# Kernel tuning notes

Measured on AMD Instinct MI355X. Metric: run time of the kernel, lower is better.

Reference implementation:

```python
import jax, jax.numpy as jnp
import numpy as np

JITTER = 0.002  # original adds 0.001*I globally plus 0.001*I on each diagonal block


def setup_inputs() -> dict:
    key = jax.random.key(0)
    k1, k2, k3 = jax.random.split(key, 3)
    T, N, D, Z = 4, 1024, 64, 4
    x = jax.random.normal(k1, (T, N, D), dtype=jnp.float32)      # per-task features
    W = jax.random.normal(k2, (T, Z), dtype=jnp.float32)         # task-to-latent mixing weights
    theta = jax.random.uniform(k3, (Z, 2), dtype=jnp.float32)    # [amplitude, inv-lengthscale] per latent GP
    return {"x": x, "W": W, "theta": theta}


def reference(x, W, theta):
    # Faithful, fused version of MTGP.rbf_kernel_mo_hete with x2=None and equal
    # task lengths. cov[mi, nj] = sum_z W[task(mi),z] W[task(nj),z] * theta[z,0]
    #   * exp(-theta[z,1]/2 * ||X[mi]-X[nj]||^2)  + JITTER on the diagonal.
    T, N, D = x.shape
    Z = theta.shape[0]
    M = T * N
    X = x.reshape(M, D)
    sq = jnp.sum(X * X, axis=-1)                                  # [M]
    sqd = jnp.maximum(sq[:, None] + sq[None, :] - 2.0 * X @ X.T, 0.0)  # [M, M]
    Wexp = jnp.repeat(W, N, axis=0)                               # [M, Z] task weight per point
    cov = JITTER * jnp.eye(M, dtype=x.dtype)
    for z in range(Z):  # small fixed loop over latent GPs
        Kz = theta[z, 0] * jnp.exp(-0.5 * theta[z, 1] * sqd)      # [M, M]
        cov = cov + (Wexp[:, z][:, None] * Wexp[:, z][None, :]) * Kz
    return cov
```

## Files before the change

kernel.cpp:

```cpp
#include <hip/hip_runtime.h>


#define M_PTS 4096
#define DIM 64
#define JITTER_F 0.002f
#define NEG_HALF_LOG2E (-0.72134752044448170f)
#define NITEM 8256
#define NBLK (NITEM / 2)

typedef __attribute__((ext_vector_type(8))) short short8v;
typedef __attribute__((ext_vector_type(4))) float f32x4;

union FragU { short8v v; uint4 u; };

__device__ __forceinline__ float fast_exp2(float x) {
#if defined(__has_builtin)
#if __has_builtin(__builtin_amdgcn_exp2f)
  return __builtin_amdgcn_exp2f(x);
#else
  return exp2f(x);
#endif
#else
  return exp2f(x);
#endif
}

__device__ __forceinline__ unsigned bfr(float x) {
  unsigned u = __float_as_uint(x);
  return (u + 0x7FFFu + ((u >> 16) & 1u)) >> 16;
}
__device__ __forceinline__ float bff(unsigned h) {
  return __uint_as_float(h << 16);
}

__global__ __launch_bounds__(256) void mtgp_pack(
    const float* __restrict__ X, unsigned short* __restrict__ Ph,
    unsigned short* __restrict__ Pl, float* __restrict__ sqn) {
  const int t = blockIdx.x * 256 + threadIdx.x;
  const int row = t >> 1, k0 = t & 1;
  const float4* xr = (const float4*)(X + (size_t)row * DIM + k0 * 32);
  float va[32];
  float s = 0.0f;
#pragma unroll
  for (int i = 0; i < 8; ++i) {
    const float4 vv = xr[i];
    va[4 * i + 0] = vv.x; va[4 * i + 1] = vv.y;
    va[4 * i + 2] = vv.z; va[4 * i + 3] = vv.w;
    s = fmaf(vv.x, vv.x, s); s = fmaf(vv.y, vv.y, s);
    s = fmaf(vv.z, vv.z, s); s = fmaf(vv.w, vv.w, s);
  }
  s += __shfl_xor(s, 1);
  if (k0 == 0) sqn[row] = s;
  const int fbase = ((row >> 4) * 2 + k0) * 512;
#pragma unroll
  for (int kg = 0; kg < 4; ++kg) {
    unsigned h[8], l[8];
#pragma unroll
    for (int j = 0; j < 4; ++j) {
      const float x0 = va[4 * kg + j], x1 = va[16 + 4 * kg + j];
      h[j] = bfr(x0);     l[j] = bfr(x0 - bff(h[j]));
      h[4 + j] = bfr(x1); l[4 + j] = bfr(x1 - bff(h[4 + j]));
    }
    const uint4 hv = make_uint4(h[0] | (h[1] << 16), h[2] | (h[3] << 16),
                                h[4] | (h[5] << 16), h[6] | (h[7] << 16));
    const uint4 lv = make_uint4(l[0] | (l[1] << 16), l[2] | (l[3] << 16),
                                l[4] | (l[5] << 16), l[6] | (l[7] << 16));
    const int lofs = fbase + (((kg << 4) + (row & 15)) << 3);
    *(uint4*)&Ph[lofs] = hv;
    *(uint4*)&Pl[lofs] = lv;
  }
}

__global__ __launch_bounds__(128, 6) void mtgp_main(
    const unsigned short* __restrict__ Ph, const unsigned short* __restrict__ Pl,
    const float* __restrict__ sqn, const float* __restrict__ W,
    const float* __restrict__ theta, float* __restrict__ out) {
  const int wid = threadIdx.x >> 6;
  const int lane = threadIdx.x & 63;
  const int item = blockIdx.x * 2 + wid;

  int u = (int)((257.0f - sqrtf((float)(66049 - 8 * item))) * 0.5f);
  if (u < 0) u = 0;
  if (u > 127) u = 127;
  while (u > 0 && u * (257 - u) / 2 > item) --u;
  while (u < 127 && (u + 1) * (256 - u) / 2 <= item) ++u;
  const int v = u + (item - u * (257 - u) / 2);
  const int gi0 = u << 5, gj0 = v << 5;

  const int r16 = lane & 15, kg = lane >> 4, kg4 = kg << 2;
  const int l8 = lane << 3;

  f32x4 acc[2][2];
#pragma unroll
  for (int p = 0; p < 2; ++p) { acc[p][0] = (f32x4)0.0f; acc[p][1] = (f32x4)0.0f; }

#pragma unroll 1
  for (int k0 = 0; k0 < 2; ++k0) {
    FragU ah[2], al[2], bh[2], bl[2];
#pragma unroll
    for (int p = 0; p < 2; ++p) {
      const int fa = ((2 * u + p) * 2 + k0) * 512 + l8;
      const int fb = ((2 * v + p) * 2 + k0) * 512 + l8;
      ah[p].u = *(const uint4*)&Ph[fa];
      al[p].u = *(const uint4*)&Pl[fa];
      bh[p].u = *(const uint4*)&Ph[fb];
      bl[p].u = *(const uint4*)&Pl[fb];
    }
#pragma unroll
    for (int p = 0; p < 2; ++p)
#pragma unroll
      for (int q = 0; q < 2; ++q) {
        acc[p][q] = __builtin_amdgcn_mfma_f32_16x16x32_bf16(ah[p].v, bh[q].v, acc[p][q], 0, 0, 0);
        acc[p][q] = __builtin_amdgcn_mfma_f32_16x16x32_bf16(ah[p].v, bl[q].v, acc[p][q], 0, 0, 0);
        acc[p][q] = __builtin_amdgcn_mfma_f32_16x16x32_bf16(al[p].v, bh[q].v, acc[p][q], 0, 0, 0);
      }
  }

  const int ti = u >> 5, tj = v >> 5;
  float czv[4], ezv[4];
#pragma unroll
  for (int z = 0; z < 4; ++z) {
    czv[z] = W[ti * 4 + z] * W[tj * 4 + z] * theta[2 * z];
    ezv[z] = NEG_HALF_LOG2E * theta[2 * z + 1];
  }
  f32x4 sqr[2];
#pragma unroll
  for (int p = 0; p < 2; ++p) sqr[p] = *(const f32x4*)&sqn[gi0 + p * 16 + kg4];
  float sqc[2];
#pragma unroll
  for (int q = 0; q < 2; ++q) sqc[q] = sqn[gj0 + q * 16 + r16];

#pragma unroll
  for (int p = 0; p < 2; ++p)
#pragma unroll
    for (int q = 0; q < 2; ++q)
#pragma unroll
      for (int rr = 0; rr < 4; ++rr) {
        const float d = acc[p][q][rr];
        const float sd = fmaxf(fmaf(-2.0f, d, sqr[p][rr] + sqc[q]), 0.0f);
        float val = czv[0] * fast_exp2(ezv[0] * sd);
        val = fmaf(czv[1], fast_exp2(ezv[1] * sd), val);
        val = fmaf(czv[2], fast_exp2(ezv[2] * sd), val);
        val = fmaf(czv[3], fast_exp2(ezv[3] * sd), val);
        if (u == v && p * 16 + kg4 + rr == q * 16 + r16) val += JITTER_F;
        acc[p][q][rr] = val;
      }

#pragma unroll
  for (int p = 0; p < 2; ++p)
#pragma unroll
    for (int rr = 0; rr < 4; ++rr) {
      float* rp = out + (size_t)(gi0 + p * 16 + kg4 + rr) * M_PTS + gj0 + r16;
      rp[0] = acc[p][0][rr];
      rp[16] = acc[p][1][rr];
    }
  if (u != v) {
#pragma unroll
    for (int q = 0; q < 2; ++q)
#pragma unroll
      for (int p = 0; p < 2; ++p) {
        f32x4* tp = (f32x4*)(out + (size_t)(gj0 + q * 16 + r16) * M_PTS + gi0 + p * 16 + kg4);
        *tp = acc[p][q];
      }
  }
}

extern "C" void kernel_launch(void* const* d_in, const int* in_sizes, int n_in,
                              void* d_out, int out_size, void* d_ws, size_t ws_size,
                              hipStream_t stream) {
  const float* x     = (const float*)d_in[0];
  const float* W     = (const float*)d_in[1];
  const float* theta = (const float*)d_in[2];
  float* out = (float*)d_out;

  float* sqn = (float*)d_ws;
  unsigned short* Ph = (unsigned short*)((char*)d_ws + 16384);
  unsigned short* Pl = (unsigned short*)((char*)d_ws + 16384 + 524288);

  mtgp_pack<<<dim3(32), dim3(256), 0, stream>>>(x, Ph, Pl, sqn);
  mtgp_main<<<dim3(NBLK), dim3(128), 0, stream>>>(Ph, Pl, sqn, W, theta, out);
}
```

Baseline: 26.95 us.

## Drop symmetric triangle tiling for full row-slab tiles with direct vector stores

Replaces the upper-triangle 32x32 tile scheme, which computed each tile once and wrote it plus its transpose, with a full-matrix layout. Each block owns a 16-row strip and a 1024-column quarter, and each wave loops over 16 column tiles. The A fragments stay in registers, and the operands are swapped so every output store is a contiguous row-major float4. This removes the strided transposed stores and the sqrt-based index decode, but doubles the MFMA and exp work because the symmetry is no longer exploited.

```diff
diff --git a/kernel.cpp b/kernel.cpp
--- a/kernel.cpp
+++ b/kernel.cpp
@@ -5,8 +5,6 @@
 #define DIM 64
 #define JITTER_F 0.002f
 #define NEG_HALF_LOG2E (-0.72134752044448170f)
-#define NITEM 8256
-#define NBLK (NITEM / 2)
 
 typedef __attribute__((ext_vector_type(8))) short short8v;
 typedef __attribute__((ext_vector_type(4))) float f32x4;
@@ -71,97 +69,70 @@
   }
 }
 
-__global__ __launch_bounds__(128, 6) void mtgp_main(
+__global__ __launch_bounds__(256, 4) void mtgp_main(
     const unsigned short* __restrict__ Ph, const unsigned short* __restrict__ Pl,
     const float* __restrict__ sqn, const float* __restrict__ W,
     const float* __restrict__ theta, float* __restrict__ out) {
-  const int wid = threadIdx.x >> 6;
-  const int lane = threadIdx.x & 63;
-  const int item = blockIdx.x * 2 + wid;
-
-  int u = (int)((257.0f - sqrtf((float)(66049 - 8 * item))) * 0.5f);
-  if (u < 0) u = 0;
-  if (u > 127) u = 127;
-  while (u > 0 && u * (257 - u) / 2 > item) --u;
-  while (u < 127 && (u + 1) * (256 - u) / 2 <= item) ++u;
-  const int v = u + (item - u * (257 - u) / 2);
-  const int gi0 = u << 5, gj0 = v << 5;
-
+  const int wid = threadIdx.x >> 6, lane = threadIdx.x & 63;
+  const int rs = blockIdx.x >> 2;
+  const int cq = blockIdx.x & 3;
+  const int row0 = rs << 4;
+  const int slab0 = cq * 64 + wid * 16;
   const int r16 = lane & 15, kg = lane >> 4, kg4 = kg << 2;
   const int l8 = lane << 3;
 
-  f32x4 acc[2][2];
-#pragma unroll
-  for (int p = 0; p < 2; ++p) { acc[p][0] = (f32x4)0.0f; acc[p][1] = (f32x4)0.0f; }
+  FragU ah0, al0, ah1, al1;
+  {
+    const int fb = (rs * 2) * 512 + l8;
+    ah0.u = *(const uint4*)&Ph[fb];
+    al0.u = *(const uint4*)&Pl[fb];
+    ah1.u = *(const uint4*)&Ph[fb + 512];
+    al1.u = *(const uint4*)&Pl[fb + 512];
+  }
+  const float sqr = sqn[row0 + r16];
 
-#pragma unroll 1
-  for (int k0 = 0; k0 < 2; ++k0) {
-    FragU ah[2], al[2], bh[2], bl[2];
-#pragma unroll
-    for (int p = 0; p < 2; ++p) {
-      const int fa = ((2 * u + p) * 2 + k0) * 512 + l8;
-      const int fb = ((2 * v + p) * 2 + k0) * 512 + l8;
-      ah[p].u = *(const uint4*)&Ph[fa];
-      al[p].u = *(const uint4*)&Pl[fa];
-      bh[p].u = *(const uint4*)&Ph[fb];
-      bl[p].u = *(const uint4*)&Pl[fb];
-    }
-#pragma unroll
-    for (int p = 0; p < 2; ++p)
-#pragma unroll
-      for (int q = 0; q < 2; ++q) {
-        acc[p][q] = __builtin_amdgcn_mfma_f32_16x16x32_bf16(ah[p].v, bh[q].v, acc[p][q], 0, 0, 0);
-        acc[p][q] = __builtin_amdgcn_mfma_f32_16x16x32_bf16(ah[p].v, bl[q].v, acc[p][q], 0, 0, 0);
-        acc[p][q] = __builtin_amdgcn_mfma_f32_16x16x32_bf16(al[p].v, bh[q].v, acc[p][q], 0, 0, 0);
-      }
-  }
-
-  const int ti = u >> 5, tj = v >> 5;
+  const int ti = rs >> 6, tj = cq;
   float czv[4], ezv[4];
 #pragma unroll
   for (int z = 0; z < 4; ++z) {
     czv[z] = W[ti * 4 + z] * W[tj * 4 + z] * theta[2 * z];
     ezv[z] = NEG_HALF_LOG2E * theta[2 * z + 1];
   }
-  f32x4 sqr[2];
-#pragma unroll
-  for (int p = 0; p < 2; ++p) sqr[p] = *(const f32x4*)&sqn[gi0 + p * 16 + kg4];
-  float sqc[2];
-#pragma unroll
-  for (int q = 0; q < 2; ++q) sqc[q] = sqn[gj0 + q * 16 + r16];
 
-#pragma unroll
-  for (int p = 0; p < 2; ++p)
-#pragma unroll
-    for (int q = 0; q < 2; ++q)
-#pragma unroll
-      for (int rr = 0; rr < 4; ++rr) {
-        const float d = acc[p][q][rr];
-        const float sd = fmaxf(fmaf(-2.0f, d, sqr[p][rr] + sqc[q]), 0.0f);
-        float val = czv[0] * fast_exp2(ezv[0] * sd);
-        val = fmaf(czv[1], fast_exp2(ezv[1] * sd), val);
-        val = fmaf(czv[2], fast_exp2(ezv[2] * sd), val);
-        val = fmaf(czv[3], fast_exp2(ezv[3] * sd), val);
-        if (u == v && p * 16 + kg4 + rr == q * 16 + r16) val += JITTER_F;
-        acc[p][q][rr] = val;
-      }
+  float* orow = out + (size_t)(row0 + r16) * M_PTS;
+  const int diag0 = row0 + r16 - kg4;
 
-#pragma unroll
-  for (int p = 0; p < 2; ++p)
+#pragma unroll 2
+  for (int s = 0; s < 16; ++s) {
+    const int v = slab0 + s;
+    const int fb = (v * 2) * 512 + l8;
+    FragU bh0, bl0, bh1, bl1;
+    bh0.u = *(const uint4*)&Ph[fb];
+    bl0.u = *(const uint4*)&Pl[fb];
+    bh1.u = *(const uint4*)&Ph[fb + 512];
+    bl1.u = *(const uint4*)&Pl[fb + 512];
+
+    f32x4 acc = (f32x4)0.0f;
+    acc = __builtin_amdgcn_mfma_f32_16x16x32_bf16(bh0.v, ah0.v, acc, 0, 0, 0);
+    acc = __builtin_amdgcn_mfma_f32_16x16x32_bf16(bh0.v, al0.v, acc, 0, 0, 0);
+    acc = __builtin_amdgcn_mfma_f32_16x16x32_bf16(bl0.v, ah0.v, acc, 0, 0, 0);
+    acc = __builtin_amdgcn_mfma_f32_16x16x32_bf16(bh1.v, ah1.v, acc, 0, 0, 0);
+    acc = __builtin_amdgcn_mfma_f32_16x16x32_bf16(bh1.v, al1.v, acc, 0, 0, 0);
+    acc = __builtin_amdgcn_mfma_f32_16x16x32_bf16(bl1.v, ah1.v, acc, 0, 0, 0);
+
+    const f32x4 sqc = *(const f32x4*)&sqn[v * 16 + kg4];
+    f32x4 res;
 #pragma unroll
     for (int rr = 0; rr < 4; ++rr) {
-      float* rp = out + (size_t)(gi0 + p * 16 + kg4 + rr) * M_PTS + gj0 + r16;
-      rp[0] = acc[p][0][rr];
-      rp[16] = acc[p][1][rr];
+      const float sd = fmaxf(fmaf(-2.0f, acc[rr], sqr + sqc[rr]), 0.0f);
+      float val = czv[0] * fast_exp2(ezv[0] * sd);
+      val = fmaf(czv[1], fast_exp2(ezv[1] * sd), val);
+      val = fmaf(czv[2], fast_exp2(ezv[2] * sd), val);
+      val = fmaf(czv[3], fast_exp2(ezv[3] * sd), val);
+      if (diag0 - v * 16 == rr) val += JITTER_F;
+      res[rr] = val;
     }
-  if (u != v) {
-#pragma unroll
-    for (int q = 0; q < 2; ++q)
-#pragma unroll
-      for (int p = 0; p < 2; ++p) {
-        f32x4* tp = (f32x4*)(out + (size_t)(gj0 + q * 16 + r16) * M_PTS + gi0 + p * 16 + kg4);
-        *tp = acc[p][q];
-      }
+    *(f32x4*)&orow[v * 16 + kg4] = res;
   }
 }
 
@@ -178,5 +149,5 @@
   unsigned short* Pl = (unsigned short*)((char*)d_ws + 16384 + 524288);
 
   mtgp_pack<<<dim3(32), dim3(256), 0, stream>>>(x, Ph, Pl, sqn);
-  mtgp_main<<<dim3(NBLK), dim3(128), 0, stream>>>(Ph, Pl, sqn, W, theta, out);
+  mtgp_main<<<dim3(1024), dim3(256), 0, stream>>>(Ph, Pl, sqn, W, theta, out);
 }
```

Result: slower. 35.68 us (+32.4%).
